# Kernel tuning notes

Measured on AMD Instinct MI355X. Metric: run time of the kernel, lower is better.

## Reference

```python
import jax, jax.numpy as jnp
import numpy as np
from jax import lax


def _l2n(t, eps=1e-12):
    n = jnp.sqrt(jnp.sum(t * t, axis=-1, keepdims=True))
    return t / jnp.maximum(n, eps)


def _ln(t, w, b, eps=1e-5):
    mu = jnp.mean(t, -1, keepdims=True)
    var = jnp.var(t, -1, keepdims=True)
    return (t - mu) / jnp.sqrt(var + eps) * w + b


def _unfold3(x):
    # nn.Unfold(kernel_size=3, padding=1, stride=1): [B,C,H,W] -> [B,C,9,H*W]
    B, C, H, W = x.shape
    xp = jnp.pad(x, ((0, 0), (0, 0), (1, 1), (1, 1)))
    pat = jnp.stack([xp[:, :, i:i + H, j:j + W] for i in range(3) for j in range(3)], axis=2)
    return pat.reshape(B, C, 9, H * W)


def _forward(x, norm1_w, norm1_b, q_w, q_b, kv_w, kv_b, temperature, query_embedding,
             learnable_tokens, learnable_bias, sr_w, sr_b, pln_w, pln_b, proj_w, proj_b,
             norm2_w, norm2_b, fc1_w, fc1_b, dw_w, dw_b, fc2_w, fc2_b):
    B, C, H, W = x.shape
    nh = temperature.shape[0]
    d = C // nh
    N = H * W
    K = 9  # local_len = window_size**2
    # norm1 (WithBias LayerNorm over channel dim, channels-last)
    y = _ln(x.reshape(B, C, N).transpose(0, 2, 1), norm1_w, norm1_b)  # [B,N,C]
    # ---- AggregatedAttention ----
    q = (y @ q_w.T + q_b).reshape(B, N, nh, d).transpose(0, 2, 1, 3)  # [B,h,N,d]
    qn = _l2n(q)
    qs = (qn + query_embedding) * jax.nn.softplus(temperature)
    kv = y @ kv_w.T + kv_b  # [B,N,2C]
    k_loc = _l2n(kv[..., :C].reshape(B, N, nh, d)).reshape(B, N, C)
    kvl = jnp.concatenate([k_loc, kv[..., C:]], -1).transpose(0, 2, 1).reshape(B, 2 * C, H, W)
    pat = _unfold3(kvl).reshape(B, 2 * nh, d, K, N).transpose(0, 1, 4, 2, 3)  # [B,2h,N,d,K]
    k_l, v_l = pat[:, :nh], pat[:, nh:]
    attn_local = jnp.einsum('bhnd,bhndk->bhnk', qs, k_l)  # [B,h,N,K]
    # pooled branch; sr_ratio=1 so adaptive_avg_pool2d is identity
    y4 = y.transpose(0, 2, 1).reshape(B, C, H, W)
    xp = jax.nn.gelu(jnp.einsum('oc,bchw->bohw', sr_w, y4) + sr_b[:, None, None], approximate=False)
    xp = _ln(xp.reshape(B, C, N).transpose(0, 2, 1), pln_w, pln_b)  # [B,pool_len,C]
    kvp = (xp @ kv_w.T + kv_b).reshape(B, N, 2 * nh, d).transpose(0, 2, 1, 3)
    k_p = _l2n(kvp[:, :nh])
    v_p = kvp[:, nh:]
    attn_pool = jnp.einsum('bhnd,bhmd->bhnm', qs, k_p)  # [B,h,N,pool_len]
    attn = jax.nn.softmax(jnp.concatenate([attn_local, attn_pool], -1), axis=-1)
    a_l, a_p = attn[..., :K], attn[..., K:]
    w_l = jnp.einsum('bhnd,hdk->bhnk', qn, learnable_tokens) + learnable_bias + a_l
    x_local = jnp.einsum('bhnk,bhndk->bhnd', w_l, v_l)
    x_pool = jnp.einsum('bhnm,bhmd->bhnd', a_p, v_p)
    xo = (x_local + x_pool).transpose(0, 2, 1, 3).reshape(B, N, C)
    # proj then raw torch-style reshape [B,N,C] -> [B,C,H,W] (memory reinterpretation)
    xo = (xo @ proj_w.T + proj_b).reshape(B, C, H, W)
    x = x + xo
    # ---- ConvolutionalGLU MLP ----
    hf = dw_b.shape[0]
    y2 = _ln(x.reshape(B, C, N).transpose(0, 2, 1), norm2_w, norm2_b).transpose(0, 2, 1).reshape(B, C, H, W)
    f1 = jnp.einsum('oc,bchw->bohw', fc1_w, y2) + fc1_b[:, None, None]
    a, v = f1[:, :hf], f1[:, hf:]
    dw = lax.conv_general_dilated(a, dw_w, (1, 1), ((1, 1), (1, 1)),
                                  feature_group_count=hf,
                                  dimension_numbers=('NCHW', 'OIHW', 'NCHW')) + dw_b[:, None, None]
    g = jax.nn.gelu(dw, approximate=False) * v
    out = jnp.einsum('oc,bchw->bohw', fc2_w, g) + fc2_b[:, None, None]
    return x + out


def setup_inputs() -> dict:
    key = jax.random.key(0)
    B, C, H, W = 2, 128, 56, 56
    nh, d, K = 4, 32, 9
    hf = int(2 * int(C * 4.0) / 3)  # 341
    ks = iter(jax.random.split(key, 16))
    rn = lambda shape, s=0.02: jax.random.normal(next(ks), shape, jnp.float32) * s
    return {
        'x': jax.random.normal(next(ks), (B, C, H, W), jnp.float32),
        'norm1_w': jnp.ones((C,), jnp.float32), 'norm1_b': jnp.zeros((C,), jnp.float32),
        'q_w': rn((C, C)), 'q_b': jnp.zeros((C,), jnp.float32),
        'kv_w': rn((2 * C, C)), 'kv_b': jnp.zeros((2 * C,), jnp.float32),
        'temperature': jnp.full((nh, 1, 1), float(np.log(np.exp(1.0 / 0.24) - 1.0)), jnp.float32),
        'query_embedding': rn((nh, 1, d)),
        'learnable_tokens': rn((nh, d, K)),
        'learnable_bias': jnp.zeros((nh, 1, K), jnp.float32),
        'sr_w': rn((C, C)), 'sr_b': jnp.zeros((C,), jnp.float32),
        'pln_w': jnp.ones((C,), jnp.float32), 'pln_b': jnp.zeros((C,), jnp.float32),
        'proj_w': rn((C, C)), 'proj_b': jnp.zeros((C,), jnp.float32),
        'norm2_w': jnp.ones((C,), jnp.float32), 'norm2_b': jnp.zeros((C,), jnp.float32),
        'fc1_w': rn((2 * hf, C)), 'fc1_b': jnp.zeros((2 * hf,), jnp.float32),
        'dw_w': rn((hf, 1, 3, 3)), 'dw_b': jnp.zeros((hf,), jnp.float32),
        'fc2_w': rn((C, hf)), 'fc2_b': jnp.zeros((C,), jnp.float32),
    }


def reference(x, norm1_w, norm1_b, q_w, q_b, kv_w, kv_b, temperature, query_embedding,
              learnable_tokens, learnable_bias, sr_w, sr_b, pln_w, pln_b, proj_w, proj_b,
              norm2_w, norm2_b, fc1_w, fc1_b, dw_w, dw_b, fc2_w, fc2_b):
    return _forward(x, norm1_w, norm1_b, q_w, q_b, kv_w, kv_b, temperature, query_embedding,
                    learnable_tokens, learnable_bias, sr_w, sr_b, pln_w, pln_b, proj_w, proj_b,
                    norm2_w, norm2_b, fc1_w, fc1_b, dw_w, dw_b, fc2_w, fc2_b)
```

## Files before the change

kernel.cpp:

```cpp
#include <hip/hip_runtime.h>
#include <hip/hip_bf16.h>

typedef __hip_bfloat16 bf16;
typedef short s8v __attribute__((ext_vector_type(8)));
typedef float f4v __attribute__((ext_vector_type(4)));

#define DEVI __device__ __forceinline__

DEVI float cvt(float x){ return x; }
DEVI float cvt(bf16 x){ return __bfloat162float(x); }

DEVI void stg(float* p, float v){ *p = v; }
DEVI void stg(bf16* p, float v){ *p = __float2bfloat16(v); }

DEVI float gelu_exact(float x){
  return 0.5f*x*(1.0f + erff(x*0.70710678118654752440f));
}

constexpr int B_ = 2, C_ = 128, H_ = 56, W_ = 56, N_ = 3136, NH_ = 4, D_ = 32, HF_ = 341;
constexpr int ROWS_ = B_*N_;
constexpr int KF2 = 352;
constexpr int GQ_ = NH_*B_*N_;
constexpr int FW = 512;
constexpr int KSP = 2;

template<typename TX, typename TY, bool PLANES>
__global__ __launch_bounds__(256)
void ln_kernel(const TX* __restrict__ x, long xstr, const float* __restrict__ w,
               const float* __restrict__ bia, TY* __restrict__ y)
{
  int gid = blockIdx.x*4 + (threadIdx.x>>6);
  int lane = threadIdx.x & 63;
  int b = gid / N_, n = gid % N_;
  float v0, v1;
  if (PLANES){
    v0 = cvt(x[((long)b*C_ + lane     )*N_ + n]);
    v1 = cvt(x[((long)b*C_ + lane + 64)*N_ + n]);
  } else {
    v0 = cvt(x[(long)gid*xstr + lane     ]);
    v1 = cvt(x[(long)gid*xstr + lane + 64]);
  }
  float s = v0+v1, ss = v0*v0 + v1*v1;
  #pragma unroll
  for (int o=32;o>0;o>>=1){ s += __shfl_xor(s,o); ss += __shfl_xor(ss,o); }
  float mu  = s*(1.0f/128.0f);
  float var = fmaxf(ss*(1.0f/128.0f) - mu*mu, 0.f);
  float inv = rsqrtf(var + 1e-5f);
  stg(&y[(long)gid*C_ + lane     ], (v0-mu)*inv*w[lane     ] + bia[lane     ]);
  stg(&y[(long)gid*C_ + lane + 64], (v1-mu)*inv*w[lane + 64] + bia[lane + 64]);
}

__global__ __launch_bounds__(256)
void convw_kernel(const float* __restrict__ q_w, const float* __restrict__ kv_w,
                  const float* __restrict__ sr_w, const float* __restrict__ proj_w,
                  const float* __restrict__ fc1_w, const float* __restrict__ fc2_w,
                  const float* __restrict__ q_b, const float* __restrict__ kv_b,
                  const float* __restrict__ sr_b,
                  bf16* __restrict__ out, float* __restrict__ bias_out)
{
  int t = blockIdx.x*256 + threadIdx.x;
  if (t >= 214272){
    int i = t - 214272;
    if (i < 512){
      float bv = (i < 128) ? q_b[i] : (i < 384) ? kv_b[i-128] : sr_b[i-384];
      bias_out[i] = bv;
    }
    return;
  }
  float v;
  if      (t <  16384) v = q_w[t];
  else if (t <  49152) v = kv_w[t-16384];
  else if (t <  65536) v = sr_w[t-49152];
  else if (t <  81920) v = proj_w[t-65536];
  else if (t < 169216) v = fc1_w[t-81920];
  else {
    int i = t - 169216; int m = i / KF2, kp = i % KF2;
    v = (kp < HF_) ? fc2_w[m*HF_ + kp] : 0.f;
  }
  out[t] = __float2bfloat16(v);
}

template<int KT, int MODE, typename TC>
__global__ __launch_bounds__(256)
void gemm_mfma(const bf16* __restrict__ A, const bf16* __restrict__ B,
               const float* __restrict__ bias, const float* __restrict__ res,
               TC* __restrict__ Cm, int M, int Nn,
               long sA, long sB, long sC, long sR)
{
  A  += (long)blockIdx.z * sA;
  B  += (long)blockIdx.z * sB;
  Cm += (long)blockIdx.z * sC;
  if (res) res += (long)blockIdx.z * sR;
  int lane = threadIdx.x & 63, w = threadIdx.x >> 6;
  int m = lane & 15, quad = lane >> 4;
  int n0 = blockIdx.x*64, m0 = blockIdx.y*64;
  int arow = m0 + w*16 + m;
  if (arow >= M) arow = M-1;
  const bf16* ap = A + (long)arow*KT + quad*8;
  const bf16* bp = B + (long)(n0 + m)*KT + quad*8;
  f4v acc[4];
  #pragma unroll
  for (int s=0;s<4;s++) acc[s] = (f4v){0.f,0.f,0.f,0.f};
  #pragma unroll
  for (int k0 = 0; k0 < KT; k0 += 32){
    s8v af = *(const s8v*)(ap + k0);
    #pragma unroll
    for (int s=0;s<4;s++){
      s8v bf = *(const s8v*)(bp + (long)s*16*KT + k0);
      acc[s] = __builtin_amdgcn_mfma_f32_16x16x32_bf16(af, bf, acc[s], 0, 0, 0);
    }
  }
  #pragma unroll
  for (int s=0;s<4;s++){
    int gn = n0 + s*16 + m;
    #pragma unroll
    for (int r=0;r<4;r++){
      int gm = m0 + w*16 + quad*4 + r;
      if (gm >= M) continue;
      float v = acc[s][r];
      if (MODE==1 || MODE==2 || MODE==4 || MODE==6) v += bias[gn];
      else                                          v += bias[gm];
      if (MODE==2) v = gelu_exact(v);
      if (MODE==6 && gn >= 384) v = gelu_exact(v);
      if (MODE==4 || MODE==5) v += res[(long)gm*Nn + gn];
      stg(&Cm[(long)gm*Nn + gn], v);
    }
  }
}

__global__ __launch_bounds__(256)
void post_q_kernel(const bf16* __restrict__ fused, const float* __restrict__ qe,
                   const float* __restrict__ temp, bf16* __restrict__ qs)
{
  int t = blockIdx.x*256 + threadIdx.x;
  int n = t % N_; int bh = t / N_; int h = bh & 3; int b = bh >> 2;
  float sp = log1pf(expf(temp[h]));
  const bf16* qr = fused + ((long)(b*N_ + n))*FW + h*D_;
  float v[32]; float ss = 0.f;
  #pragma unroll
  for (int d=0;d<32;d++){ v[d] = cvt(qr[d]); ss = fmaf(v[d], v[d], ss); }
  float inv = 1.f/fmaxf(sqrtf(ss), 1e-12f);
  bf16* qo = qs + ((long)bh*N_ + n)*D_;
  #pragma unroll
  for (int d=0;d<32;d++)
    stg(&qo[d], (v[d]*inv + qe[h*D_+d])*sp);
}

__global__ __launch_bounds__(256)
void post_kvp_kernel(const bf16* __restrict__ kvp_raw,
                     bf16* __restrict__ kp, bf16* __restrict__ vp)
{
  int t = blockIdx.x*256 + threadIdx.x;
  int n = t % N_; int bh = t / N_; int h = bh & 3; int b = bh >> 2;
  const bf16* kr = kvp_raw + ((long)(b*N_ + n))*(2*C_) + h*D_;
  float v[32]; float ss = 0.f;
  #pragma unroll
  for (int d=0;d<32;d++){ v[d] = cvt(kr[d]); ss = fmaf(v[d], v[d], ss); }
  float inv = 1.f/fmaxf(sqrtf(ss), 1e-12f);
  bf16* ko = kp + ((long)bh*N_ + n)*D_;
  #pragma unroll
  for (int d=0;d<32;d++) stg(&ko[d], v[d]*inv);
  #pragma unroll
  for (int d=0;d<32;d++) vp[((long)bh*D_ + d)*N_ + n] = kr[C_ + d];
}

__global__ __launch_bounds__(256)
void attn_part_kernel(const bf16* __restrict__ qs_, const bf16* __restrict__ kp_,
                      const bf16* __restrict__ vp_,
                      bf16* __restrict__ Op, float* __restrict__ Lp)
{
  int bh = blockIdx.y;
  int z  = blockIdx.z;
  int lane = threadIdx.x & 63;
  int w    = threadIdx.x >> 6;
  int m    = lane & 15, quad = lane >> 4;
  int qA   = blockIdx.x*128 + w*16;
  int qB   = qA + 64;
  bool hasB = (qB < N_);
  __shared__ float sm[4][1184];
  bf16*  PA   = (bf16*)sm[w];
  bf16*  PB   = PA + 1152;
  float* Olds = sm[w];

  s8v afA = *(const s8v*)(qs_ + ((long)bh*N_ + qA + m)*D_ + quad*8);
  s8v afB = hasB ? *(const s8v*)(qs_ + ((long)bh*N_ + qB + m)*D_ + quad*8) : afA;
  const bf16* kpb = kp_ + (long)bh*N_*D_;
  const bf16* vpb = vp_ + (long)bh*D_*N_;
  f4v oA0={0.f,0.f,0.f,0.f}, oA1={0.f,0.f,0.f,0.f};
  f4v oB0={0.f,0.f,0.f,0.f}, oB1={0.f,0.f,0.f,0.f};
  float lA[4]={0.f,0.f,0.f,0.f}, lB[4]={0.f,0.f,0.f,0.f};

  int tlo = z*1600, thi = min(tlo + 1600, N_);
  for (int t0 = tlo; t0 < thi; t0 += 64){
    s8v kf[4], vf[4];
    #pragma unroll
    for (int s=0;s<4;s++)
      kf[s] = *(const s8v*)(kpb + (long)(t0 + s*16 + m)*D_ + quad*8);
    vf[0] = *(const s8v*)(vpb + (long)(m     )*N_ + t0      + quad*8);
    vf[1] = *(const s8v*)(vpb + (long)(16 + m)*N_ + t0      + quad*8);
    vf[2] = *(const s8v*)(vpb + (long)(m     )*N_ + t0 + 32 + quad*8);
    vf[3] = *(const s8v*)(vpb + (long)(16 + m)*N_ + t0 + 32 + quad*8);
    #pragma unroll
    for (int s = 0; s < 4; s++){
      f4v cA = {0.f,0.f,0.f,0.f}, cB = {0.f,0.f,0.f,0.f};
      cA = __builtin_amdgcn_mfma_f32_16x16x32_bf16(afA, kf[s], cA, 0, 0, 0);
      cB = __builtin_amdgcn_mfma_f32_16x16x32_bf16(afB, kf[s], cB, 0, 0, 0);
      #pragma unroll
      for (int r=0;r<4;r++){
        float eA = __expf(cA[r] - 8.f);
        float eB = __expf(cB[r] - 8.f);
        lA[r] += eA; lB[r] += eB;
        PA[(quad*4+r)*72 + s*16 + m] = __float2bfloat16(eA);
        PB[(quad*4+r)*72 + s*16 + m] = __float2bfloat16(eB);
      }
    }
    #pragma unroll
    for (int c2=0;c2<2;c2++){
      s8v paA = *(const s8v*)(PA + m*72 + c2*32 + quad*8);
      s8v paB = *(const s8v*)(PB + m*72 + c2*32 + quad*8);
      oA0 = __builtin_amdgcn_mfma_f32_16x16x32_bf16(paA, vf[c2*2  ], oA0, 0, 0, 0);
      oA1 = __builtin_amdgcn_mfma_f32_16x16x32_bf16(paA, vf[c2*2+1], oA1, 0, 0, 0);
      oB0 = __builtin_amdgcn_mfma_f32_16x16x32_bf16(paB, vf[c2*2  ], oB0, 0, 0, 0);
      oB1 = __builtin_amdgcn_mfma_f32_16x16x32_bf16(paB, vf[c2*2+1], oB1, 0, 0, 0);
    }
  }
  #pragma unroll
  for (int ph=0; ph<2; ph++){
    if (ph == 1 && !hasB) break;
    float* lacc = ph ? lB : lA;
    f4v    o0   = ph ? oB0 : oA0;
    f4v    o1   = ph ? oB1 : oA1;
    int    qq   = ph ? qB  : qA;
    float lr[4] = {lacc[0], lacc[1], lacc[2], lacc[3]};
    #pragma unroll
    for (int off=1; off<16; off<<=1)
      #pragma unroll
      for (int r=0;r<4;r++) lr[r] += __shfl_xor(lr[r], off);
    #pragma unroll
    for (int r=0;r<4;r++){
      Olds[(quad*4+r)*36 + m     ] = o0[r];
      Olds[(quad*4+r)*36 + 16 + m] = o1[r];
    }
    if (m == 0){
      #pragma unroll
      for (int r=0;r<4;r++) Olds[576 + quad*4 + r] = lr[r];
    }
    long gq = (long)bh*N_ + qq + m;
    f4v ov0 = *(const f4v*)(Olds + m*36 + quad*8);
    f4v ov1 = *(const f4v*)(Olds + m*36 + quad*8 + 4);
    bf16 o8[8];
    #pragma unroll
    for (int j=0;j<4;j++){ o8[j] = __float2bfloat16(ov0[j]); o8[4+j] = __float2bfloat16(ov1[j]); }
    *(s8v*)(Op + ((long)z*GQ_ + gq)*32 + quad*8) = *(const s8v*)o8;
    if (quad == 0) Lp[(long)z*GQ_ + gq] = Olds[576 + m];
  }
}

__global__ __launch_bounds__(256)
void attn_combine_kernel(const bf16* __restrict__ Op, const float* __restrict__ Lp,
                         const bf16* __restrict__ qs_, const bf16* __restrict__ fused,
                         const float* __restrict__ qe, const float* __restrict__ temp,
                         const float* __restrict__ tokens, const float* __restrict__ tbias,
                         bf16* __restrict__ xo)
{
  int gq = blockIdx.x*256 + threadIdx.x;
  int n = gq % N_; int bh = gq / N_; int h = bh & 3; int b = bh >> 2;
  float L = 0.f;
  float out[32];
  #pragma unroll
  for (int d=0;d<32;d++) out[d] = 0.f;
  #pragma unroll
  for (int z=0; z<KSP; z++){
    L += Lp[(long)z*GQ_ + gq];
    const bf16* oz = Op + ((long)z*GQ_ + gq)*32;
    #pragma unroll
    for (int d=0;d<32;d++) out[d] += cvt(oz[d]);
  }
  const bf16* qrow = qs_ + (long)gq*D_;
  float q[32];
  #pragma unroll
  for (int d=0;d<32;d++) q[d] = cvt(qrow[d]);
  int hy = n / W_, wx = n % W_;
  const bf16* kvb = fused + (long)b*N_*FW + 128 + h*D_;
  float sl[9];
  #pragma unroll
  for (int k=0;k<9;k++){
    int di = k/3-1, dj = k%3-1;
    int yy = hy+di, xx = wx+dj;
    float s = 0.f;
    if (yy>=0 && yy<H_ && xx>=0 && xx<W_){
      long nn2 = (long)(yy*W_+xx)*FW;
      float dot = 0.f, ss = 0.f;
      #pragma unroll
      for (int d=0;d<32;d++){
        float kk = cvt(kvb[nn2 + d]);
        dot = fmaf(q[d], kk, dot);
        ss  = fmaf(kk, kk, ss);
      }
      s = dot / fmaxf(sqrtf(ss), 1e-12f);
    }
    sl[k] = s;
  }
  #pragma unroll
  for (int k=0;k<9;k++) L += __expf(sl[k] - 8.f);
  float invL = 1.f/L;
  #pragma unroll
  for (int d=0;d<32;d++) out[d] *= invL;
  float sp = log1pf(expf(temp[h]));
  float invsp = 1.f/sp;
  float qn[32];
  #pragma unroll
  for (int d=0;d<32;d++) qn[d] = q[d]*invsp - qe[h*D_+d];
  #pragma unroll
  for (int k=0;k<9;k++){
    float tok = 0.f;
    #pragma unroll
    for (int d=0;d<32;d++) tok = fmaf(qn[d], tokens[(h*D_+d)*9+k], tok);
    float wl = tok + tbias[h*9+k] + __expf(sl[k] - 8.f)*invL;
    int di = k/3-1, dj = k%3-1;
    int yy = hy+di, xx = wx+dj;
    if (yy>=0 && yy<H_ && xx>=0 && xx<W_){
      long nn2 = (long)(yy*W_+xx)*FW;
      #pragma unroll
      for (int d=0;d<32;d++) out[d] = fmaf(wl, cvt(kvb[nn2 + 128 + d]), out[d]);
    }
  }
  bf16* op = xo + ((long)(b*N_ + n))*C_ + h*D_;
  #pragma unroll
  for (int d=0;d<32;d++) stg(&op[d], out[d]);
}

__global__ __launch_bounds__(256)
void dwconv_kernel(const bf16* __restrict__ f1, const float* __restrict__ dww,
                   const float* __restrict__ dwb, bf16* __restrict__ g)
{
  int t = blockIdx.x*256 + threadIdx.x;
  if (t >= B_*N_*44) return;
  int b = t / (N_*44); int r = t - b*(N_*44);
  int n = r % N_, cg = r / N_;
  f1 += (long)b*2*HF_*N_;
  g  += (long)b*N_*KF2;
  int c0 = cg*8;
  int hy = n / W_, wx = n % W_;
  bf16 o8[8];
  #pragma unroll
  for (int j=0;j<8;j++){
    int c = c0 + j;
    float val = 0.f;
    if (c < HF_){
      const bf16* ap = f1 + (long)c*N_;
      float s = dwb[c];
      #pragma unroll
      for (int di=-1; di<=1; di++)
        #pragma unroll
        for (int dj=-1; dj<=1; dj++){
          int yy = hy+di, xx = wx+dj;
          if (yy>=0 && yy<H_ && xx>=0 && xx<W_)
            s = fmaf(dww[c*9 + (di+1)*3 + (dj+1)], cvt(ap[yy*W_+xx]), s);
        }
      val = gelu_exact(s) * cvt(f1[(long)(HF_+c)*N_ + n]);
    }
    o8[j] = __float2bfloat16(val);
  }
  *(s8v*)(g + (long)n*KF2 + c0) = *(const s8v*)o8;
}

extern "C" void kernel_launch(void* const* d_in, const int* in_sizes, int n_in,
                              void* d_out, int out_size, void* d_ws, size_t ws_size,
                              hipStream_t stream)
{
  (void)in_sizes; (void)n_in; (void)out_size; (void)ws_size;
  const float* x_in      = (const float*)d_in[0];
  const float* norm1_w   = (const float*)d_in[1];
  const float* norm1_b   = (const float*)d_in[2];
  const float* q_w       = (const float*)d_in[3];
  const float* q_b       = (const float*)d_in[4];
  const float* kv_w      = (const float*)d_in[5];
  const float* kv_b      = (const float*)d_in[6];
  const float* temp      = (const float*)d_in[7];
  const float* qe        = (const float*)d_in[8];
  const float* tokens    = (const float*)d_in[9];
  const float* tbias     = (const float*)d_in[10];
  const float* sr_w      = (const float*)d_in[11];
  const float* sr_b      = (const float*)d_in[12];
  const float* pln_w     = (const float*)d_in[13];
  const float* pln_b     = (const float*)d_in[14];
  const float* proj_w    = (const float*)d_in[15];
  const float* proj_b    = (const float*)d_in[16];
  const float* norm2_w   = (const float*)d_in[17];
  const float* norm2_b   = (const float*)d_in[18];
  const float* fc1_w     = (const float*)d_in[19];
  const float* fc1_b     = (const float*)d_in[20];
  const float* dw_w      = (const float*)d_in[21];
  const float* dw_b      = (const float*)d_in[22];
  const float* fc2_w     = (const float*)d_in[23];
  const float* fc2_b     = (const float*)d_in[24];

  char* w8 = (char*)d_ws;
  bf16*  fused   = (bf16*)(w8 + 0);
  float* x2      = (float*)(w8 + 0);
  bf16*  y2      = (bf16*)(w8 + 3211264);
  bf16*  f1b     = (bf16*)(w8 + 4816896);
  bf16*  qs      = (bf16*)(w8 + 6422528);
  bf16*  xp      = (bf16*)(w8 + 8028160);
  bf16*  k_p     = (bf16*)(w8 + 8028160);
  bf16*  v_p     = (bf16*)(w8 + 9633792);
  bf16*  kvp_raw = (bf16*)(w8 + 11239424);
  bf16*  Opart   = (bf16*)(w8 + 11239424);
  bf16*  g_rows  = (bf16*)(w8 + 17661952);
  bf16*  wbase   = (bf16*)(w8 + 22077440);
  float* fbias   = (float*)(w8 + 22505984);
  bf16*  y       = f1b;
  bf16*  xo      = (bf16*)d_out;
  float* Lpart   = (float*)((char*)d_out + 1605632);
  bf16*  proj_wb = wbase + 65536;
  bf16*  fc1_wb  = wbase + 81920;
  bf16*  fc2_wb  = wbase + 169216;

  convw_kernel<<<(214784+255)/256, 256, 0, stream>>>(
      q_w, kv_w, sr_w, proj_w, fc1_w, fc2_w, q_b, kv_b, sr_b, wbase, fbias);
  ln_kernel<float, bf16, true><<<ROWS_/4, 256, 0, stream>>>(x_in, 0, norm1_w, norm1_b, y);
  gemm_mfma<128, 6, bf16><<<dim3(8,98), 256, 0, stream>>>(
      y, wbase, fbias, nullptr, fused, ROWS_, FW, 0,0,0,0);
  post_q_kernel<<<98, 256, 0, stream>>>(fused, qe, temp, qs);
  ln_kernel<bf16, bf16, false><<<ROWS_/4, 256, 0, stream>>>(fused + 384, FW, pln_w, pln_b, xp);
  gemm_mfma<128, 1, bf16><<<dim3(4,98), 256, 0, stream>>>(
      xp, wbase + 16384, kv_b, nullptr, kvp_raw, ROWS_, 256, 0,0,0,0);
  post_kvp_kernel<<<98, 256, 0, stream>>>(kvp_raw, k_p, v_p);
  attn_part_kernel<<<dim3(25,8,KSP), 256, 0, stream>>>(qs, k_p, v_p, Opart, Lpart);
  attn_combine_kernel<<<GQ_/256, 256, 0, stream>>>(Opart, Lpart, qs, fused,
                                                   qe, temp, tokens, tbias, xo);
  gemm_mfma<128, 4, float><<<dim3(2,98), 256, 0, stream>>>(
      xo, proj_wb, proj_b, x_in, x2, ROWS_, 128, 0,0,0,0);
  ln_kernel<float, bf16, true><<<ROWS_/4, 256, 0, stream>>>(x2, 0, norm2_w, norm2_b, y2);
  gemm_mfma<128, 3, bf16><<<dim3(49,11,B_), 256, 0, stream>>>(
      fc1_wb, y2, fc1_b, nullptr, f1b, 2*HF_, N_,
      0, (long)N_*C_, (long)2*HF_*N_, 0);
  dwconv_kernel<<<(B_*N_*44+255)/256, 256, 0, stream>>>(f1b, dw_w, dw_b, g_rows);
  gemm_mfma<KF2, 5, float><<<dim3(49,2,B_), 256, 0, stream>>>(
      fc2_wb, g_rows, fc2_b, x2, (float*)d_out, C_, N_,
      0, (long)N_*KF2, (long)C_*N_, (long)C_*N_);
}
```

Measured before the change: 270.2 us.

## Process four query chunks per wave in attention and split keys four ways

Each wave in the partial-attention kernel now computes four 16-row query tiles instead of two, so every K/V fragment loaded from global memory is reused across four MFMA query tiles. To keep enough blocks in flight, the key range is split into four parts instead of two, and the grid becomes 13x8x4. The intent is to cut redundant K/V global loads per query. In exchange, per-wave registers and LDS grow (more accumulators, a 36 KB shared buffer), which may reduce occupancy, and the combine step now merges twice as many partial results.

```diff
diff --git a/kernel.cpp b/kernel.cpp
--- a/kernel.cpp
+++ b/kernel.cpp
@@ -22,7 +22,7 @@
 constexpr int KF2 = 352;
 constexpr int GQ_ = NH_*B_*N_;
 constexpr int FW = 512;
-constexpr int KSP = 2;
+constexpr int KSP = 4;
 
 template<typename TX, typename TY, bool PLANES>
 __global__ __launch_bounds__(256)
@@ -174,23 +174,30 @@
   int lane = threadIdx.x & 63;
   int w    = threadIdx.x >> 6;
   int m    = lane & 15, quad = lane >> 4;
-  int qA   = blockIdx.x*128 + w*16;
-  int qB   = qA + 64;
-  bool hasB = (qB < N_);
-  __shared__ float sm[4][1184];
-  bf16*  PA   = (bf16*)sm[w];
-  bf16*  PB   = PA + 1152;
+  int base = blockIdx.x*256 + w*16;
+  __shared__ float sm[4][2304];
+  bf16*  Pl   = (bf16*)sm[w];
   float* Olds = sm[w];
 
-  s8v afA = *(const s8v*)(qs_ + ((long)bh*N_ + qA + m)*D_ + quad*8);
-  s8v afB = hasB ? *(const s8v*)(qs_ + ((long)bh*N_ + qB + m)*D_ + quad*8) : afA;
+  s8v af[4]; bool hasQ[4];
+  #pragma unroll
+  for (int ch=0; ch<4; ch++){
+    int qq = base + ch*64;
+    hasQ[ch] = (qq < N_);
+    af[ch] = *(const s8v*)(qs_ + ((long)bh*N_ + (hasQ[ch] ? qq : base) + m)*D_ + quad*8);
+  }
   const bf16* kpb = kp_ + (long)bh*N_*D_;
   const bf16* vpb = vp_ + (long)bh*D_*N_;
-  f4v oA0={0.f,0.f,0.f,0.f}, oA1={0.f,0.f,0.f,0.f};
-  f4v oB0={0.f,0.f,0.f,0.f}, oB1={0.f,0.f,0.f,0.f};
-  float lA[4]={0.f,0.f,0.f,0.f}, lB[4]={0.f,0.f,0.f,0.f};
-
-  int tlo = z*1600, thi = min(tlo + 1600, N_);
+  f4v o0[4], o1[4];
+  float l[4][4];
+  #pragma unroll
+  for (int ch=0; ch<4; ch++){
+    o0[ch] = (f4v){0.f,0.f,0.f,0.f}; o1[ch] = (f4v){0.f,0.f,0.f,0.f};
+    #pragma unroll
+    for (int r=0;r<4;r++) l[ch][r] = 0.f;
+  }
+
+  int tlo = z*768, thi = (z==3) ? N_ : tlo + 768;
   for (int t0 = tlo; t0 < thi; t0 += 64){
     s8v kf[4], vf[4];
     #pragma unroll
@@ -202,50 +209,46 @@
     vf[3] = *(const s8v*)(vpb + (long)(16 + m)*N_ + t0 + 32 + quad*8);
     #pragma unroll
     for (int s = 0; s < 4; s++){
-      f4v cA = {0.f,0.f,0.f,0.f}, cB = {0.f,0.f,0.f,0.f};
-      cA = __builtin_amdgcn_mfma_f32_16x16x32_bf16(afA, kf[s], cA, 0, 0, 0);
-      cB = __builtin_amdgcn_mfma_f32_16x16x32_bf16(afB, kf[s], cB, 0, 0, 0);
-      #pragma unroll
-      for (int r=0;r<4;r++){
-        float eA = __expf(cA[r] - 8.f);
-        float eB = __expf(cB[r] - 8.f);
-        lA[r] += eA; lB[r] += eB;
-        PA[(quad*4+r)*72 + s*16 + m] = __float2bfloat16(eA);
-        PB[(quad*4+r)*72 + s*16 + m] = __float2bfloat16(eB);
+      #pragma unroll
+      for (int ch=0; ch<4; ch++){
+        f4v c = {0.f,0.f,0.f,0.f};
+        c = __builtin_amdgcn_mfma_f32_16x16x32_bf16(af[ch], kf[s], c, 0, 0, 0);
+        #pragma unroll
+        for (int r=0;r<4;r++){
+          float e = __expf(c[r] - 8.f);
+          l[ch][r] += e;
+          Pl[ch*1152 + (quad*4+r)*72 + s*16 + m] = __float2bfloat16(e);
+        }
       }
     }
     #pragma unroll
     for (int c2=0;c2<2;c2++){
-      s8v paA = *(const s8v*)(PA + m*72 + c2*32 + quad*8);
-      s8v paB = *(const s8v*)(PB + m*72 + c2*32 + quad*8);
-      oA0 = __builtin_amdgcn_mfma_f32_16x16x32_bf16(paA, vf[c2*2  ], oA0, 0, 0, 0);
-      oA1 = __builtin_amdgcn_mfma_f32_16x16x32_bf16(paA, vf[c2*2+1], oA1, 0, 0, 0);
-      oB0 = __builtin_amdgcn_mfma_f32_16x16x32_bf16(paB, vf[c2*2  ], oB0, 0, 0, 0);
-      oB1 = __builtin_amdgcn_mfma_f32_16x16x32_bf16(paB, vf[c2*2+1], oB1, 0, 0, 0);
-    }
-  }
-  #pragma unroll
-  for (int ph=0; ph<2; ph++){
-    if (ph == 1 && !hasB) break;
-    float* lacc = ph ? lB : lA;
-    f4v    o0   = ph ? oB0 : oA0;
-    f4v    o1   = ph ? oB1 : oA1;
-    int    qq   = ph ? qB  : qA;
-    float lr[4] = {lacc[0], lacc[1], lacc[2], lacc[3]};
+      #pragma unroll
+      for (int ch=0; ch<4; ch++){
+        s8v pa = *(const s8v*)(Pl + ch*1152 + m*72 + c2*32 + quad*8);
+        o0[ch] = __builtin_amdgcn_mfma_f32_16x16x32_bf16(pa, vf[c2*2  ], o0[ch], 0, 0, 0);
+        o1[ch] = __builtin_amdgcn_mfma_f32_16x16x32_bf16(pa, vf[c2*2+1], o1[ch], 0, 0, 0);
+      }
+    }
+  }
+  #pragma unroll
+  for (int ch=0; ch<4; ch++){
+    if (!hasQ[ch]) continue;
+    float lr[4] = {l[ch][0], l[ch][1], l[ch][2], l[ch][3]};
     #pragma unroll
     for (int off=1; off<16; off<<=1)
       #pragma unroll
       for (int r=0;r<4;r++) lr[r] += __shfl_xor(lr[r], off);
     #pragma unroll
     for (int r=0;r<4;r++){
-      Olds[(quad*4+r)*36 + m     ] = o0[r];
-      Olds[(quad*4+r)*36 + 16 + m] = o1[r];
+      Olds[(quad*4+r)*36 + m     ] = o0[ch][r];
+      Olds[(quad*4+r)*36 + 16 + m] = o1[ch][r];
     }
     if (m == 0){
       #pragma unroll
       for (int r=0;r<4;r++) Olds[576 + quad*4 + r] = lr[r];
     }
-    long gq = (long)bh*N_ + qq + m;
+    long gq = (long)bh*N_ + base + ch*64 + m;
     f4v ov0 = *(const f4v*)(Olds + m*36 + quad*8);
     f4v ov1 = *(const f4v*)(Olds + m*36 + quad*8 + 4);
     bf16 o8[8];
@@ -427,7 +430,7 @@
   gemm_mfma<128, 1, bf16><<<dim3(4,98), 256, 0, stream>>>(
       xp, wbase + 16384, kv_b, nullptr, kvp_raw, ROWS_, 256, 0,0,0,0);
   post_kvp_kernel<<<98, 256, 0, stream>>>(kvp_raw, k_p, v_p);
-  attn_part_kernel<<<dim3(25,8,KSP), 256, 0, stream>>>(qs, k_p, v_p, Opart, Lpart);
+  attn_part_kernel<<<dim3(13,8,KSP), 256, 0, stream>>>(qs, k_p, v_p, Opart, Lpart);
   attn_combine_kernel<<<GQ_/256, 256, 0, stream>>>(Opart, Lpart, qs, fused,
                                                    qe, temp, tokens, tbias, xo);
   gemm_mfma<128, 4, float><<<dim3(2,98), 256, 0, stream>>>(
```

New measurement: 272.3 us. Within noise of the previous version (+0.8%).
